# Kernel optimization log

Hardware: AMD Instinct MI355X
Metric: run time of the kernel (lower is better)

The kernel has to match this reference:

```python
import math
import jax, jax.numpy as jnp
import numpy as np

STRESS_MAGNITUDE = 72000000.0
H = 0.01
C = 3.5e-12
N_LAMBDA = 371


def setup_inputs() -> dict:
    key = jax.random.key(0)
    k1, k2 = jax.random.split(key)
    stressmap = jax.random.normal(k1, (8, 1, 1024, 1024), dtype=jnp.float32)
    ss_interaction = jax.random.uniform(k2, (N_LAMBDA, 3), dtype=jnp.float32)
    return {"stressmap": stressmap, "ss_interaction": ss_interaction}


def reference(stressmap, ss_interaction):
    # stressmap: [bs, 1, rows, cols]; ss_interaction: [371, 3]
    stress_in = jnp.squeeze(stressmap, axis=1)  # [bs, rows, cols]
    mn = stress_in.min(axis=(1, 2), keepdims=True)
    mx = stress_in.max(axis=(1, 2), keepdims=True)
    stress_nomal = (stress_in - mn) / (mx - mn)
    stress_real = stress_nomal * STRESS_MAGNITUDE

    lam = jnp.linspace(390.0, 760.0, N_LAMBDA, dtype=jnp.float32)  # nm
    coef = 2.0 * math.pi * H * C / 1e-9  # phase = coef * stress / lambda_nm

    bs, rows, cols = stress_real.shape
    iso0 = jnp.zeros((bs, 3, rows, cols), dtype=stress_real.dtype)

    def step(acc, xs):
        l_i, w_i = xs  # scalar wavelength, [3] interaction row
        phase = (coef / l_i) * stress_real            # [bs, rows, cols]
        term = 0.5 * (1.0 - jnp.cos(phase))           # [bs, rows, cols]
        acc = acc + w_i[None, :, None, None] * term[:, None, :, :]
        return acc, None

    isochromatic, _ = jax.lax.scan(step, iso0, (lam, ss_interaction))
    iso_fringe = isochromatic / isochromatic.max(axis=(1, 2, 3), keepdims=True)
    return iso_fringe, stress_nomal
```

## Files before the change

kernel.cpp:

```cpp
#include <hip/hip_runtime.h>
#include <math.h>

#define NL 371
#define LUTN 1024
#define NPIX (1024*1024)
#define NB 8
#define K1B 64
#define NBIN 1024
#define VLO -8.0f
#define BINSCALE 64.0f
#define WV 0.015625f
#define STRESS_MAG 72000000.0f

__device__ __forceinline__ void lut_interp(const float4* slut, float s,
                                           float& i0, float& i1, float& i2) {
    float t = s * (float)(LUTN - 1);
    int j = (int)t;
    j = min(j, LUTN - 2);
    float fr = t - (float)j;
    float4 A = slut[j];
    float4 B = slut[j + 1];
    i0 = fmaf(fr, B.x - A.x, A.x);
    i1 = fmaf(fr, B.y - A.y, A.y);
    i2 = fmaf(fr, B.z - A.z, A.z);
}

__global__ __launch_bounds__(256) void k_stage1(const float4* __restrict__ x,
                                                const float* __restrict__ w,
                                                float4* __restrict__ lutg,
                                                float2* __restrict__ partials,
                                                unsigned* __restrict__ bitmaps) {
    __shared__ unsigned ubuf[2272];
    const int tid = threadIdx.x;
    const int bx  = blockIdx.x;

    if (bx < NB * K1B) {
        unsigned* sflag = ubuf;
        float* smn = (float*)(ubuf + 256);
        float* smx = smn + 4;
        sflag[tid] = 0u;
        __syncthreads();
        int b = bx >> 6, blk = bx & 63;
        const float4* p = x + (size_t)b * (NPIX / 4);
        unsigned char* f = (unsigned char*)sflag;
        float mn = 3.4e38f, mx = -3.4e38f;
        for (int i = blk * 256 + tid; i < NPIX / 4; i += K1B * 256) {
            float4 v = p[i];
            mn = fminf(mn, fminf(fminf(v.x, v.y), fminf(v.z, v.w)));
            mx = fmaxf(mx, fmaxf(fmaxf(v.x, v.y), fmaxf(v.z, v.w)));
            int b0 = min(NBIN - 1, max(0, (int)((v.x - VLO) * BINSCALE)));
            int b1 = min(NBIN - 1, max(0, (int)((v.y - VLO) * BINSCALE)));
            int b2 = min(NBIN - 1, max(0, (int)((v.z - VLO) * BINSCALE)));
            int b3 = min(NBIN - 1, max(0, (int)((v.w - VLO) * BINSCALE)));
            f[b0] = 1; f[b1] = 1; f[b2] = 1; f[b3] = 1;
        }
        for (int off = 32; off >= 1; off >>= 1) {
            mn = fminf(mn, __shfl_down(mn, off));
            mx = fmaxf(mx, __shfl_down(mx, off));
        }
        int wid = tid >> 6;
        if ((tid & 63) == 0) { smn[wid] = mn; smx[wid] = mx; }
        __syncthreads();
        if (tid < 32) {
            unsigned m = 0;
            for (int k = 0; k < 32; ++k) m |= (f[tid * 32 + k] ? 1u : 0u) << k;
            bitmaps[(size_t)(b * K1B + blk) * 32 + tid] = m;
        }
        if (tid == 0) {
            for (int k = 1; k < 4; ++k) { mn = fminf(mn, smn[k]); mx = fmaxf(mx, smx[k]); }
            partials[b * K1B + blk] = make_float2(mn, mx);
        }
    } else {
        float* kw = (float*)ubuf;
        float* w0 = kw + NL; float* w1 = w0 + NL; float* w2 = w1 + NL;
        float* rr = w2 + NL;
        const float coef_rev = (float)(0.01 * 3.5e-12 / 1e-9) * STRESS_MAG;
        for (int i = tid; i < NL; i += 256) {
            float lam = 390.0f + (float)i;
            kw[i] = coef_rev / lam;
            w0[i] = w[i * 3 + 0]; w1[i] = w[i * 3 + 1]; w2[i] = w[i * 3 + 2];
        }
        __syncthreads();
        int jj = tid & 15, part = tid >> 4;
        int j  = (bx - NB * K1B) * 16 + jj;
        float s = (float)j * (1.0f / (float)(LUTN - 1));
        float a0 = 0.f, a1 = 0.f, a2 = 0.f;
        for (int i = part; i < NL; i += 16) {
            float r = kw[i] * s;
            r = r - floorf(r);
            float c = __builtin_amdgcn_cosf(r);
            float t = fmaf(-0.5f, c, 0.5f);
            a0 = fmaf(w0[i], t, a0); a1 = fmaf(w1[i], t, a1); a2 = fmaf(w2[i], t, a2);
        }
        rr[tid] = a0; rr[256 + tid] = a1; rr[512 + tid] = a2;
        __syncthreads();
        if (part == 0) {
            float s0 = 0.f, s1 = 0.f, s2 = 0.f;
            for (int p2 = 0; p2 < 16; ++p2) {
                s0 += rr[p2 * 16 + jj];
                s1 += rr[256 + p2 * 16 + jj];
                s2 += rr[512 + p2 * 16 + jj];
            }
            lutg[j] = make_float4(s0, s1, s2, 0.0f);
        }
    }
}

__global__ __launch_bounds__(256) void k_stage2(const float4* __restrict__ x,
                                                const float4* __restrict__ lutg,
                                                const float2* __restrict__ partials,
                                                const unsigned* __restrict__ bitmaps,
                                                float4* __restrict__ snorm,
                                                float4* __restrict__ iso) {
    __shared__ float4 slut[LUTN];
    __shared__ unsigned socc[32];
    __shared__ float sP[4];
    __shared__ float sm[4];
    const int tid = threadIdx.x;
    const int b = blockIdx.y;
    for (int i = tid; i < LUTN; i += 256) slut[i] = lutg[i];
    if (tid < 64) {
        float2 pm = partials[b * K1B + tid];
        float mn = pm.x, mx = pm.y;
        for (int off = 32; off >= 1; off >>= 1) {
            mn = fminf(mn, __shfl_down(mn, off));
            mx = fmaxf(mx, __shfl_down(mx, off));
        }
        if (tid == 0) { sP[0] = mn; sP[1] = mx; }
    } else if (tid < 96) {
        int k = tid - 64;
        unsigned m = 0;
        for (int blk = 0; blk < K1B; ++blk)
            m |= bitmaps[(size_t)(b * K1B + blk) * 32 + k];
        socc[k] = m;
    }
    __syncthreads();
    float mn = sP[0], mx = sP[1];
    float inv = 1.0f / (mx - mn);

    float mloc = 0.0f;
    for (int bin = tid; bin < NBIN; bin += 256) {
        if ((socc[bin >> 5] >> (bin & 31)) & 1u) {
            float vlo = VLO + (float)bin * WV;
            float sa = fminf(1.0f, fmaxf(0.0f, (vlo - mn) * inv));
            float sb = fminf(1.0f, fmaxf(0.0f, (vlo + WV - mn) * inv));
            float i0, i1, i2;
            lut_interp(slut, sa, i0, i1, i2);
            mloc = fmaxf(mloc, fmaxf(fmaxf(i0, i1), i2));
            lut_interp(slut, sb, i0, i1, i2);
            mloc = fmaxf(mloc, fmaxf(fmaxf(i0, i1), i2));
            int ja = (int)(sa * (float)(LUTN - 1));
            int jb = min((int)(sb * (float)(LUTN - 1)), LUTN - 1);
            for (int j = ja + 1; j <= jb; ++j) {
                float4 A = slut[j];
                mloc = fmaxf(mloc, fmaxf(fmaxf(A.x, A.y), A.z));
            }
        }
    }
    for (int off = 32; off >= 1; off >>= 1)
        mloc = fmaxf(mloc, __shfl_down(mloc, off));
    int wid = tid >> 6;
    if ((tid & 63) == 0) sm[wid] = mloc;
    __syncthreads();
    if (tid == 0) sP[2] = fmaxf(fmaxf(sm[0], sm[1]), fmaxf(sm[2], sm[3]));
    __syncthreads();
    float invIso = 1.0f / sP[2];

    const float4* p = x + (size_t)b * (NPIX / 4);
    float4* qs = snorm + (size_t)b * (NPIX / 4);
    float4* q0 = iso + (size_t)(b * 3 + 0) * (NPIX / 4);
    float4* q1 = iso + (size_t)(b * 3 + 1) * (NPIX / 4);
    float4* q2 = iso + (size_t)(b * 3 + 2) * (NPIX / 4);
    for (int i = blockIdx.x * 256 + tid; i < NPIX / 4; i += gridDim.x * 256) {
        float4 v = p[i];
        float4 s;
        s.x = (v.x - mn) * inv; s.y = (v.y - mn) * inv;
        s.z = (v.z - mn) * inv; s.w = (v.w - mn) * inv;
        qs[i] = s;
        float4 r0, r1, r2;
        float i0, i1, i2;
        lut_interp(slut, s.x, i0, i1, i2);
        r0.x = i0 * invIso; r1.x = i1 * invIso; r2.x = i2 * invIso;
        lut_interp(slut, s.y, i0, i1, i2);
        r0.y = i0 * invIso; r1.y = i1 * invIso; r2.y = i2 * invIso;
        lut_interp(slut, s.z, i0, i1, i2);
        r0.z = i0 * invIso; r1.z = i1 * invIso; r2.z = i2 * invIso;
        lut_interp(slut, s.w, i0, i1, i2);
        r0.w = i0 * invIso; r1.w = i1 * invIso; r2.w = i2 * invIso;
        q0[i] = r0; q1[i] = r1; q2[i] = r2;
    }
}

extern "C" void kernel_launch(void* const* d_in, const int* in_sizes, int n_in,
                              void* d_out, int out_size, void* d_ws, size_t ws_size,
                              hipStream_t stream) {
    const float4* x = (const float4*)d_in[0];
    const float*  w = (const float*)d_in[1];

    float* out    = (float*)d_out;
    float4* iso   = (float4*)out;
    float4* snorm = (float4*)(out + (size_t)NB * 3 * NPIX);

    float4*   lutg     = (float4*)d_ws;
    float2*   partials = (float2*)((char*)d_ws + 16384);
    unsigned* bitmaps  = (unsigned*)((char*)d_ws + 16384 + 4096);

    k_stage1<<<dim3(NB * K1B + LUTN / 16), dim3(256), 0, stream>>>(
        x, w, lutg, partials, bitmaps);
    k_stage2<<<dim3(128, NB), dim3(256), 0, stream>>>(
        x, lutg, partials, bitmaps, snorm, iso);
}
```

Measured before the change: 51.24 us.

## Split per-batch constant reduction into its own kernel and use nontemporal stores

The per-batch min/max and iso-maximum reduction, previously repeated by every one of the 1024 stage-2 blocks, moves into a small 8-block kernel that writes the constants to workspace. The streaming stage-2 kernel then just loads those constants. Its output writes (normalized stress and the three iso channels) become nontemporal stores to reduce cache pollution. This adds a third kernel launch and a serialization point between stages.

```diff
diff --git a/kernel.cpp b/kernel.cpp
--- a/kernel.cpp
+++ b/kernel.cpp
@@ -11,6 +11,12 @@
 #define BINSCALE 64.0f
 #define WV 0.015625f
 #define STRESS_MAG 72000000.0f
+
+typedef float v4f __attribute__((ext_vector_type(4)));
+
+__device__ __forceinline__ void store_nt(float4* p, float4 v) {
+    __builtin_nontemporal_store(*(const v4f*)&v, (v4f*)p);
+}
 
 __device__ __forceinline__ void lut_interp(const float4* slut, float s,
                                            float& i0, float& i1, float& i2) {
@@ -106,18 +112,15 @@
     }
 }
 
-__global__ __launch_bounds__(256) void k_stage2(const float4* __restrict__ x,
-                                                const float4* __restrict__ lutg,
-                                                const float2* __restrict__ partials,
-                                                const unsigned* __restrict__ bitmaps,
-                                                float4* __restrict__ snorm,
-                                                float4* __restrict__ iso) {
+__global__ __launch_bounds__(256) void k_const(const float4* __restrict__ lutg,
+                                               const float2* __restrict__ partials,
+                                               const unsigned* __restrict__ bitmaps,
+                                               float4* __restrict__ consts) {
     __shared__ float4 slut[LUTN];
     __shared__ unsigned socc[32];
-    __shared__ float sP[4];
-    __shared__ float sm[4];
+    __shared__ float red[8];
     const int tid = threadIdx.x;
-    const int b = blockIdx.y;
+    const int b = blockIdx.x;
     for (int i = tid; i < LUTN; i += 256) slut[i] = lutg[i];
     if (tid < 64) {
         float2 pm = partials[b * K1B + tid];
@@ -126,7 +129,7 @@
             mn = fminf(mn, __shfl_down(mn, off));
             mx = fmaxf(mx, __shfl_down(mx, off));
         }
-        if (tid == 0) { sP[0] = mn; sP[1] = mx; }
+        if (tid == 0) { red[0] = mn; red[1] = mx; }
     } else if (tid < 96) {
         int k = tid - 64;
         unsigned m = 0;
@@ -135,7 +138,7 @@
         socc[k] = m;
     }
     __syncthreads();
-    float mn = sP[0], mx = sP[1];
+    float mn = red[0], mx = red[1];
     float inv = 1.0f / (mx - mn);
 
     float mloc = 0.0f;
@@ -160,11 +163,26 @@
     for (int off = 32; off >= 1; off >>= 1)
         mloc = fmaxf(mloc, __shfl_down(mloc, off));
     int wid = tid >> 6;
-    if ((tid & 63) == 0) sm[wid] = mloc;
+    if ((tid & 63) == 0) red[4 + wid] = mloc;
     __syncthreads();
-    if (tid == 0) sP[2] = fmaxf(fmaxf(sm[0], sm[1]), fmaxf(sm[2], sm[3]));
+    if (tid == 0) {
+        float isoM = fmaxf(fmaxf(red[4], red[5]), fmaxf(red[6], red[7]));
+        consts[b] = make_float4(mn, inv, 1.0f / isoM, 0.0f);
+    }
+}
+
+__global__ __launch_bounds__(256) void k_stage2(const float4* __restrict__ x,
+                                                const float4* __restrict__ lutg,
+                                                const float4* __restrict__ consts,
+                                                float4* __restrict__ snorm,
+                                                float4* __restrict__ iso) {
+    __shared__ float4 slut[LUTN];
+    const int tid = threadIdx.x;
+    const int b = blockIdx.y;
+    for (int i = tid; i < LUTN; i += 256) slut[i] = lutg[i];
+    float4 cb = consts[b];
+    float mn = cb.x, inv = cb.y, invIso = cb.z;
     __syncthreads();
-    float invIso = 1.0f / sP[2];
 
     const float4* p = x + (size_t)b * (NPIX / 4);
     float4* qs = snorm + (size_t)b * (NPIX / 4);
@@ -176,7 +194,7 @@
         float4 s;
         s.x = (v.x - mn) * inv; s.y = (v.y - mn) * inv;
         s.z = (v.z - mn) * inv; s.w = (v.w - mn) * inv;
-        qs[i] = s;
+        store_nt(&qs[i], s);
         float4 r0, r1, r2;
         float i0, i1, i2;
         lut_interp(slut, s.x, i0, i1, i2);
@@ -187,7 +205,9 @@
         r0.z = i0 * invIso; r1.z = i1 * invIso; r2.z = i2 * invIso;
         lut_interp(slut, s.w, i0, i1, i2);
         r0.w = i0 * invIso; r1.w = i1 * invIso; r2.w = i2 * invIso;
-        q0[i] = r0; q1[i] = r1; q2[i] = r2;
+        store_nt(&q0[i], r0);
+        store_nt(&q1[i], r1);
+        store_nt(&q2[i], r2);
     }
 }
 
@@ -204,9 +224,11 @@
     float4*   lutg     = (float4*)d_ws;
     float2*   partials = (float2*)((char*)d_ws + 16384);
     unsigned* bitmaps  = (unsigned*)((char*)d_ws + 16384 + 4096);
+    float4*   consts   = (float4*)((char*)d_ws + 16384 + 4096 + 65536);
 
     k_stage1<<<dim3(NB * K1B + LUTN / 16), dim3(256), 0, stream>>>(
         x, w, lutg, partials, bitmaps);
+    k_const<<<dim3(NB), dim3(256), 0, stream>>>(lutg, partials, bitmaps, consts);
     k_stage2<<<dim3(128, NB), dim3(256), 0, stream>>>(
-        x, lutg, partials, bitmaps, snorm, iso);
-}
+        x, lutg, consts, snorm, iso);
+}
```

Result: slower. 54.20 us (+5.8%).
